# Performance work log

Hardware: AMD Instinct MI355X
Metric: run time of the kernel (lower is better)

Reference implementation:

```python
import jax, jax.numpy as jnp
import numpy as np

EMBED = 384
HEAD = 64


def setup_inputs() -> dict:
    key = jax.random.key(0)
    kx, kq, kk, kv = jax.random.split(key, 4)
    B, T = 4, 4096
    x = jax.random.normal(kx, (B, T, EMBED), dtype=jnp.float32)
    # torch Linear(384, 64, bias=False): weight (64, 384), y = x @ W.T.
    # Store pre-transposed as (EMBED, HEAD) so y = x @ W.
    s = 1.0 / np.sqrt(EMBED)  # kaiming-uniform-ish scale
    Wq = jax.random.uniform(kq, (EMBED, HEAD), jnp.float32, -s, s)
    Wk = jax.random.uniform(kk, (EMBED, HEAD), jnp.float32, -s, s)
    Wv = jax.random.uniform(kv, (EMBED, HEAD), jnp.float32, -s, s)
    return {"x": x, "Wq": Wq, "Wk": Wk, "Wv": Wv}


def reference(x, Wq, Wk, Wv):
    # q, k, v: [B, T, H]
    q = x @ Wq
    k = x @ Wk
    v = x @ Wv
    scale = k.shape[-1] ** (-0.5)
    scores = jnp.einsum("bth,bsh->bts", q, k) * scale  # [B, T, T]
    # Faithful to the original: tril, then mask anything equal to 0 with -inf
    # (this also masks exact zeros inside the causal region).
    tril = jnp.tril(scores)
    masked = jnp.where(tril == 0, -jnp.inf, tril)
    attn = jax.nn.softmax(masked, axis=-1)
    out = jnp.einsum("bts,bsh->bth", attn, v)  # [B, T, H]
    return out
```

## Files before the change

kernel.cpp:

```cpp
#include <hip/hip_runtime.h>
#include <hip/hip_bf16.h>
#include <stdint.h>


#define EMBED 384
#define HEAD  64
#define NB    4
#define NT    4096
#define NROWS (NB * NT)
#define MAXCH 16

#define SCALE_Q 0.18033688011112042f

typedef short bf16x8 __attribute__((ext_vector_type(8)));
typedef float f32x4  __attribute__((ext_vector_type(4)));

__device__ __forceinline__ unsigned short bfround(float f) {
    union { float f; unsigned u; } v; v.f = f;
    return (unsigned short)((v.u + 0x8000u) >> 16);
}
__device__ __forceinline__ unsigned packbf(float lo, float hi) {
    union { float f; unsigned u; } a, b; a.f = lo; b.f = hi;
    return ((a.u + 0x8000u) >> 16) | ((b.u + 0x8000u) & 0xFFFF0000u);
}

__global__ __launch_bounds__(256)
void wprep_kernel(const float* __restrict__ Wq,
                  const float* __restrict__ Wk,
                  const float* __restrict__ Wv,
                  unsigned short* __restrict__ Wt)
{
    int idx = blockIdx.x * 256 + threadIdx.x;
    int k = idx / 192;
    int n = idx - k * 192;
    int sel = n >> 6, nc = n & 63;
    const float* wp = (sel == 0) ? Wq : ((sel == 1) ? Wk : Wv);
    Wt[n * EMBED + k] = bfround(wp[(size_t)k * HEAD + nc]);
}

__global__ __launch_bounds__(256, 4)
void proj_kernel(const float* __restrict__ x,
                 const unsigned short* __restrict__ Wt,
                 unsigned short* __restrict__ Qo,
                 unsigned short* __restrict__ Ko,
                 unsigned short* __restrict__ Vto)
{
    __shared__ __attribute__((aligned(16))) unsigned short wsm[192][72];
    __shared__ __attribute__((aligned(16))) unsigned short xs[64][72];
    unsigned short (*vbuf)[72] = (unsigned short (*)[72])&xs[0][0];

    const int t    = threadIdx.x;
    const int w    = t >> 6;
    const int lane = t & 63;
    const int quad = lane >> 4;
    const int l16  = lane & 15;
    const int r0   = blockIdx.x * 64;

    f32x4 acc[12];
#pragma unroll
    for (int i = 0; i < 12; ++i) acc[i] = (f32x4){0.f, 0.f, 0.f, 0.f};

    const int wrow = t >> 3, wc = t & 7;
    const int xrow = t >> 4, xc = t & 15;

    for (int kc = 0; kc < 6; ++kc) {
        const int k0 = kc * 64;
        uint4 wr[6];
#pragma unroll
        for (int i = 0; i < 6; ++i)
            wr[i] = *(const uint4*)(Wt + (size_t)(wrow + i * 32) * EMBED + k0 + wc * 8);
        float4 xr[4];
#pragma unroll
        for (int i = 0; i < 4; ++i)
            xr[i] = *(const float4*)(x + (size_t)(r0 + xrow + i * 16) * EMBED + k0 + xc * 4);
        __syncthreads();
#pragma unroll
        for (int i = 0; i < 6; ++i)
            *(uint4*)&wsm[wrow + i * 32][wc * 8] = wr[i];
#pragma unroll
        for (int i = 0; i < 4; ++i) {
            uint2 pw; pw.x = packbf(xr[i].x, xr[i].y); pw.y = packbf(xr[i].z, xr[i].w);
            *(uint2*)&xs[xrow + i * 16][xc * 4] = pw;
        }
        __syncthreads();
#pragma unroll
        for (int ks = 0; ks < 2; ++ks) {
            bf16x8 a = *(const bf16x8*)&xs[w * 16 + l16][ks * 32 + quad * 8];
#pragma unroll
            for (int nt = 0; nt < 12; ++nt) {
                bf16x8 b = *(const bf16x8*)&wsm[nt * 16 + l16][ks * 32 + quad * 8];
                acc[nt] = __builtin_amdgcn_mfma_f32_16x16x32_bf16(a, b, acc[nt], 0, 0, 0);
            }
        }
    }

#pragma unroll
    for (int nt = 0; nt < 8; ++nt) {
        int col = (nt & 3) * 16 + l16;
#pragma unroll
        for (int r = 0; r < 4; ++r) {
            int row = r0 + w * 16 + quad * 4 + r;
            if (nt < 4) Qo[(size_t)row * HEAD + col] = bfround(acc[nt][r] * SCALE_Q);
            else        Ko[(size_t)row * HEAD + col] = bfround(acc[nt][r]);
        }
    }
    __syncthreads();
#pragma unroll
    for (int nt = 8; nt < 12; ++nt) {
        int d = (nt & 3) * 16 + l16;
#pragma unroll
        for (int r = 0; r < 4; ++r)
            vbuf[d][w * 16 + quad * 4 + r] = bfround(acc[nt][r]);
    }
    __syncthreads();
    {
        const int batch = r0 >> 12;
        const int s0 = r0 & (NT - 1);
#pragma unroll
        for (int i = 0; i < 2; ++i) {
            int idx = t + i * 256;
            int d = idx >> 3, c = idx & 7;
            *(uint4*)(Vto + ((size_t)(batch * HEAD + d)) * NT + s0 + c * 8) =
                *(const uint4*)&vbuf[d][c * 8];
        }
    }
}

__global__ __launch_bounds__(256, 6)
void attn_kernel(const unsigned short* __restrict__ Qi,
                 const unsigned short* __restrict__ Ki,
                 const unsigned short* __restrict__ Vti,
                 float* __restrict__ opart,
                 float* __restrict__ lpart)
{
    __shared__ __attribute__((aligned(16))) unsigned short Kt[64][64];
    __shared__ __attribute__((aligned(16))) unsigned short Vs[64][64];
    __shared__ __attribute__((aligned(16))) unsigned short Ps[4][16][72];

    const int t    = threadIdx.x;
    const int w    = t >> 6;
    const int lane = t & 63;
    const int quad = lane >> 4;
    const int l16  = lane & 15;
    const int sw   = l16 & 7;

    const int batch = blockIdx.x & 3;
    int bid = blockIdx.x >> 2;
    int m = 63;
    int nc = 16;
    while (bid >= nc) { bid -= nc; --m; nc = (m >> 2) + 1; }
    const int c = bid;
    const int kt0 = c * 4;
    const int ntiles = min(4, m + 1 - kt0);
    const int q0 = m * 64 + w * 16;

    const unsigned short* Kbg = Ki  + (size_t)batch * NT * HEAD;
    const unsigned short* Vbg = Vti + (size_t)batch * HEAD * NT;

    bf16x8 bq0, bq1;
    {
        const unsigned short* qp = Qi + (size_t)(batch * NT + q0 + l16) * HEAD + quad * 8;
        bq0 = *(const bf16x8*)(qp);
        bq1 = *(const bf16x8*)(qp + 32);
    }

    f32x4 o[4];
#pragma unroll
    for (int i = 0; i < 4; ++i) o[i] = (f32x4){0.f, 0.f, 0.f, 0.f};
    float rs = 0.f;

    const int srow0 = t >> 3, sc = t & 7;
    const int srow1 = srow0 + 32;
    const int scc0 = sc ^ (srow0 & 7);
    const int scc1 = sc ^ (srow1 & 7);

    uint4 kr0, kr1, vr0, vr1;
    kr0 = *(const uint4*)(Kbg + (size_t)(kt0 * 64 + srow0) * HEAD + sc * 8);
    kr1 = *(const uint4*)(Kbg + (size_t)(kt0 * 64 + srow1) * HEAD + sc * 8);
    vr0 = *(const uint4*)(Vbg + (size_t)srow0 * NT + kt0 * 64 + sc * 8);
    vr1 = *(const uint4*)(Vbg + (size_t)srow1 * NT + kt0 * 64 + sc * 8);

    for (int j = 0; j < ntiles; ++j) {
        const int kt = kt0 + j;
        __syncthreads();
        *(uint4*)&Kt[srow0][scc0 * 8] = kr0;
        *(uint4*)&Kt[srow1][scc1 * 8] = kr1;
        *(uint4*)&Vs[srow0][scc0 * 8] = vr0;
        *(uint4*)&Vs[srow1][scc1 * 8] = vr1;
        __syncthreads();
        if (j + 1 < ntiles) {
            const int nt4 = (kt + 1) * 64;
            kr0 = *(const uint4*)(Kbg + (size_t)(nt4 + srow0) * HEAD + sc * 8);
            kr1 = *(const uint4*)(Kbg + (size_t)(nt4 + srow1) * HEAD + sc * 8);
            vr0 = *(const uint4*)(Vbg + (size_t)srow0 * NT + nt4 + sc * 8);
            vr1 = *(const uint4*)(Vbg + (size_t)srow1 * NT + nt4 + sc * 8);
        }

        const bool diag = (kt == m);
#pragma unroll
        for (int ts = 0; ts < 4; ++ts) {
            bf16x8 ak0 = *(const bf16x8*)&Kt[ts * 16 + l16][(quad ^ sw) * 8];
            bf16x8 ak1 = *(const bf16x8*)&Kt[ts * 16 + l16][((4 + quad) ^ sw) * 8];
            f32x4 z = (f32x4){0.f, 0.f, 0.f, 0.f};
            z = __builtin_amdgcn_mfma_f32_16x16x32_bf16(ak0, bq0, z, 0, 0, 0);
            z = __builtin_amdgcn_mfma_f32_16x16x32_bf16(ak1, bq1, z, 0, 0, 0);
            float p[4];
#pragma unroll
            for (int r = 0; r < 4; ++r) {
                float pv = __builtin_amdgcn_exp2f(z[r]);
                if (diag) {
                    int sg = ts * 16 + quad * 4 + r;
                    int qg = w * 16 + l16;
                    pv = (sg > qg) ? 0.f : pv;
                }
                p[r] = pv;
            }
            rs += (p[0] + p[1]) + (p[2] + p[3]);
            uint2 pw; pw.x = packbf(p[0], p[1]); pw.y = packbf(p[2], p[3]);
            *(uint2*)&Ps[w][l16][ts * 16 + quad * 4] = pw;
        }
        bf16x8 ap0 = *(const bf16x8*)&Ps[w][l16][quad * 8];
        bf16x8 ap1 = *(const bf16x8*)&Ps[w][l16][32 + quad * 8];
#pragma unroll
        for (int nd = 0; nd < 4; ++nd) {
            bf16x8 av0 = *(const bf16x8*)&Vs[nd * 16 + l16][(quad ^ sw) * 8];
            bf16x8 av1 = *(const bf16x8*)&Vs[nd * 16 + l16][((4 + quad) ^ sw) * 8];
            o[nd] = __builtin_amdgcn_mfma_f32_16x16x32_bf16(ap0, av0, o[nd], 0, 0, 0);
            o[nd] = __builtin_amdgcn_mfma_f32_16x16x32_bf16(ap1, av1, o[nd], 0, 0, 0);
        }
    }

    rs += __shfl_xor(rs, 16, 64);
    rs += __shfl_xor(rs, 32, 64);
    if (quad == 0)
        lpart[(size_t)c * NROWS + batch * NT + q0 + l16] = rs;
    float* ob = opart + (size_t)c * NROWS * HEAD;
#pragma unroll
    for (int r = 0; r < 4; ++r) {
        size_t off = (size_t)(batch * NT + q0 + quad * 4 + r) * HEAD;
#pragma unroll
        for (int nd = 0; nd < 4; ++nd)
            ob[off + nd * 16 + l16] = o[nd][r];
    }
}

__global__ __launch_bounds__(256)
void combine_kernel(const float* __restrict__ opart,
                    const float* __restrict__ lpart,
                    float* __restrict__ out)
{
    int gid = blockIdx.x * 256 + threadIdx.x;
    int row = gid >> 4;
    int d4  = (gid & 15) * 4;
    int m   = (row & (NT - 1)) >> 6;
    int nch = (m >> 2) + 1;
    f32x4 a = (f32x4){0.f, 0.f, 0.f, 0.f};
    float l = 0.f;
    for (int cc = 0; cc < nch; ++cc) {
        a += *(const f32x4*)(opart + (size_t)cc * NROWS * HEAD + (size_t)row * HEAD + d4);
        l += lpart[(size_t)cc * NROWS + row];
    }
    float inv = 1.0f / l;
    a[0] *= inv; a[1] *= inv; a[2] *= inv; a[3] *= inv;
    *(f32x4*)(out + (size_t)row * HEAD + d4) = a;
}

extern "C" void kernel_launch(void* const* d_in, const int* in_sizes, int n_in,
                              void* d_out, int out_size, void* d_ws, size_t ws_size,
                              hipStream_t stream)
{
    const float* x  = (const float*)d_in[0];
    const float* Wq = (const float*)d_in[1];
    const float* Wk = (const float*)d_in[2];
    const float* Wv = (const float*)d_in[3];
    float* out = (float*)d_out;

    unsigned short* Qw  = (unsigned short*)d_ws;
    unsigned short* Kw  = Qw + (size_t)NROWS * HEAD;
    unsigned short* Vtw = Kw + (size_t)NROWS * HEAD;
    unsigned short* Wtw = Vtw + (size_t)NROWS * HEAD;
    float* opart = (float*)(Wtw + (size_t)192 * EMBED);
    float* lpart = opart + (size_t)MAXCH * NROWS * HEAD;

    wprep_kernel<<<(192 * EMBED) / 256, 256, 0, stream>>>(Wq, Wk, Wv, Wtw);
    proj_kernel<<<NROWS / 64, 256, 0, stream>>>(x, Wtw, Qw, Kw, Vtw);
    attn_kernel<<<4 * 544, 256, 0, stream>>>(Qw, Kw, Vtw, opart, lpart);
    combine_kernel<<<NROWS * 16 / 256, 256, 0, stream>>>(opart, lpart, out);
}
```

Baseline: 129.0 us.

## Process 128-row query tiles per block and store partial outputs in bf16

Each attention block now covers 128 query rows, with each wave handling two 16-row sub-tiles. K and V fragments are loaded from LDS once and reused for both sub-tiles, and the grid is halved. Partial output accumulators are written as bf16 instead of fp32 to cut split-K write and read traffic, and the combine kernel reads them with 8-wide loads. The cost is more registers per thread (occupancy hint lowered from 6 to 4), coarser causal work balance, and some precision loss in the partial sums.

Measured after the change: 206.4 us. 1.6x slower.

```diff
diff --git a/kernel.cpp b/kernel.cpp
--- a/kernel.cpp
+++ b/kernel.cpp
@@ -126,11 +126,11 @@
     }
 }
 
-__global__ __launch_bounds__(256, 6)
+__global__ __launch_bounds__(256, 4)
 void attn_kernel(const unsigned short* __restrict__ Qi,
                  const unsigned short* __restrict__ Ki,
                  const unsigned short* __restrict__ Vti,
-                 float* __restrict__ opart,
+                 unsigned short* __restrict__ opart,
                  float* __restrict__ lpart)
 {
     __shared__ __attribute__((aligned(16))) unsigned short Kt[64][64];
@@ -146,28 +146,31 @@
 
     const int batch = blockIdx.x & 3;
     int bid = blockIdx.x >> 2;
-    int m = 63;
-    int nc = 16;
-    while (bid >= nc) { bid -= nc; --m; nc = (m >> 2) + 1; }
+    int m = 31;
+    int nch = 16;
+    while (bid >= nch) { bid -= nch; --m; nch = (m + 2) >> 1; }
     const int c = bid;
     const int kt0 = c * 4;
-    const int ntiles = min(4, m + 1 - kt0);
-    const int q0 = m * 64 + w * 16;
+    const int ntiles = min(4, 2 * m + 2 - kt0);
+    const int qw = m * 128 + w * 32;
 
     const unsigned short* Kbg = Ki  + (size_t)batch * NT * HEAD;
     const unsigned short* Vbg = Vti + (size_t)batch * HEAD * NT;
 
-    bf16x8 bq0, bq1;
-    {
-        const unsigned short* qp = Qi + (size_t)(batch * NT + q0 + l16) * HEAD + quad * 8;
-        bq0 = *(const bf16x8*)(qp);
-        bq1 = *(const bf16x8*)(qp + 32);
-    }
-
-    f32x4 o[4];
-#pragma unroll
-    for (int i = 0; i < 4; ++i) o[i] = (f32x4){0.f, 0.f, 0.f, 0.f};
-    float rs = 0.f;
+    bf16x8 bq0[2], bq1[2];
+#pragma unroll
+    for (int qs = 0; qs < 2; ++qs) {
+        const unsigned short* qp = Qi + (size_t)(batch * NT + qw + qs * 16 + l16) * HEAD + quad * 8;
+        bq0[qs] = *(const bf16x8*)(qp);
+        bq1[qs] = *(const bf16x8*)(qp + 32);
+    }
+
+    f32x4 o[2][4];
+#pragma unroll
+    for (int a = 0; a < 2; ++a)
+#pragma unroll
+        for (int b = 0; b < 4; ++b) o[a][b] = (f32x4){0.f, 0.f, 0.f, 0.f};
+    float rs[2] = {0.f, 0.f};
 
     const int srow0 = t >> 3, sc = t & 7;
     const int srow1 = srow0 + 32;
@@ -196,73 +199,111 @@
             vr1 = *(const uint4*)(Vbg + (size_t)srow1 * NT + nt4 + sc * 8);
         }
 
-        const bool diag = (kt == m);
+        bf16x8 ak0[4], ak1[4], av0[4], av1[4];
 #pragma unroll
         for (int ts = 0; ts < 4; ++ts) {
-            bf16x8 ak0 = *(const bf16x8*)&Kt[ts * 16 + l16][(quad ^ sw) * 8];
-            bf16x8 ak1 = *(const bf16x8*)&Kt[ts * 16 + l16][((4 + quad) ^ sw) * 8];
-            f32x4 z = (f32x4){0.f, 0.f, 0.f, 0.f};
-            z = __builtin_amdgcn_mfma_f32_16x16x32_bf16(ak0, bq0, z, 0, 0, 0);
-            z = __builtin_amdgcn_mfma_f32_16x16x32_bf16(ak1, bq1, z, 0, 0, 0);
-            float p[4];
+            ak0[ts] = *(const bf16x8*)&Kt[ts * 16 + l16][(quad ^ sw) * 8];
+            ak1[ts] = *(const bf16x8*)&Kt[ts * 16 + l16][((4 + quad) ^ sw) * 8];
+        }
+#pragma unroll
+        for (int nd = 0; nd < 4; ++nd) {
+            av0[nd] = *(const bf16x8*)&Vs[nd * 16 + l16][(quad ^ sw) * 8];
+            av1[nd] = *(const bf16x8*)&Vs[nd * 16 + l16][((4 + quad) ^ sw) * 8];
+        }
+
+        const bool diag = (kt >= 2 * m);
+#pragma unroll
+        for (int qs = 0; qs < 2; ++qs) {
+            f32x4 z[4];
+#pragma unroll
+            for (int ts = 0; ts < 4; ++ts) {
+                f32x4 zz = (f32x4){0.f, 0.f, 0.f, 0.f};
+                zz = __builtin_amdgcn_mfma_f32_16x16x32_bf16(ak0[ts], bq0[qs], zz, 0, 0, 0);
+                zz = __builtin_amdgcn_mfma_f32_16x16x32_bf16(ak1[ts], bq1[qs], zz, 0, 0, 0);
+                z[ts] = zz;
+            }
+            const int qg = qw + qs * 16 + l16;
+#pragma unroll
+            for (int ts = 0; ts < 4; ++ts) {
+                float p[4];
+#pragma unroll
+                for (int r = 0; r < 4; ++r) {
+                    float pv = __builtin_amdgcn_exp2f(z[ts][r]);
+                    if (diag) {
+                        int sg = kt * 64 + ts * 16 + quad * 4 + r;
+                        pv = (sg > qg) ? 0.f : pv;
+                    }
+                    p[r] = pv;
+                }
+                rs[qs] += (p[0] + p[1]) + (p[2] + p[3]);
+                uint2 pw; pw.x = packbf(p[0], p[1]); pw.y = packbf(p[2], p[3]);
+                *(uint2*)&Ps[w][l16][ts * 16 + quad * 4] = pw;
+            }
+            bf16x8 ap0 = *(const bf16x8*)&Ps[w][l16][quad * 8];
+            bf16x8 ap1 = *(const bf16x8*)&Ps[w][l16][32 + quad * 8];
+#pragma unroll
+            for (int nd = 0; nd < 4; ++nd) {
+                o[qs][nd] = __builtin_amdgcn_mfma_f32_16x16x32_bf16(ap0, av0[nd], o[qs][nd], 0, 0, 0);
+                o[qs][nd] = __builtin_amdgcn_mfma_f32_16x16x32_bf16(ap1, av1[nd], o[qs][nd], 0, 0, 0);
+            }
+        }
+    }
+
+#pragma unroll
+    for (int qs = 0; qs < 2; ++qs) {
+        float vs = rs[qs];
+        vs += __shfl_xor(vs, 16, 64);
+        vs += __shfl_xor(vs, 32, 64);
+        if (quad == 0)
+            lpart[(size_t)c * NROWS + batch * NT + qw + qs * 16 + l16] = vs;
+    }
+    unsigned short* ob = opart + (size_t)c * NROWS * HEAD + (size_t)batch * NT * HEAD;
+#pragma unroll
+    for (int qs = 0; qs < 2; ++qs)
+#pragma unroll
+        for (int nd = 0; nd < 4; ++nd)
 #pragma unroll
             for (int r = 0; r < 4; ++r) {
-                float pv = __builtin_amdgcn_exp2f(z[r]);
-                if (diag) {
-                    int sg = ts * 16 + quad * 4 + r;
-                    int qg = w * 16 + l16;
-                    pv = (sg > qg) ? 0.f : pv;
+                float own = o[qs][nd][r];
+                float oth = __shfl_xor(own, 1, 64);
+                unsigned u = (lane & 1) ? packbf(oth, own) : packbf(own, oth);
+                if (!(lane & 1)) {
+                    int row = qw + qs * 16 + quad * 4 + r;
+                    *(unsigned*)&ob[(size_t)row * HEAD + nd * 16 + l16] = u;
                 }
-                p[r] = pv;
-            }
-            rs += (p[0] + p[1]) + (p[2] + p[3]);
-            uint2 pw; pw.x = packbf(p[0], p[1]); pw.y = packbf(p[2], p[3]);
-            *(uint2*)&Ps[w][l16][ts * 16 + quad * 4] = pw;
-        }
-        bf16x8 ap0 = *(const bf16x8*)&Ps[w][l16][quad * 8];
-        bf16x8 ap1 = *(const bf16x8*)&Ps[w][l16][32 + quad * 8];
-#pragma unroll
-        for (int nd = 0; nd < 4; ++nd) {
-            bf16x8 av0 = *(const bf16x8*)&Vs[nd * 16 + l16][(quad ^ sw) * 8];
-            bf16x8 av1 = *(const bf16x8*)&Vs[nd * 16 + l16][((4 + quad) ^ sw) * 8];
-            o[nd] = __builtin_amdgcn_mfma_f32_16x16x32_bf16(ap0, av0, o[nd], 0, 0, 0);
-            o[nd] = __builtin_amdgcn_mfma_f32_16x16x32_bf16(ap1, av1, o[nd], 0, 0, 0);
-        }
-    }
-
-    rs += __shfl_xor(rs, 16, 64);
-    rs += __shfl_xor(rs, 32, 64);
-    if (quad == 0)
-        lpart[(size_t)c * NROWS + batch * NT + q0 + l16] = rs;
-    float* ob = opart + (size_t)c * NROWS * HEAD;
-#pragma unroll
-    for (int r = 0; r < 4; ++r) {
-        size_t off = (size_t)(batch * NT + q0 + quad * 4 + r) * HEAD;
-#pragma unroll
-        for (int nd = 0; nd < 4; ++nd)
-            ob[off + nd * 16 + l16] = o[nd][r];
-    }
+            }
 }
 
 __global__ __launch_bounds__(256)
-void combine_kernel(const float* __restrict__ opart,
+void combine_kernel(const unsigned short* __restrict__ opart,
                     const float* __restrict__ lpart,
                     float* __restrict__ out)
 {
     int gid = blockIdx.x * 256 + threadIdx.x;
-    int row = gid >> 4;
-    int d4  = (gid & 15) * 4;
-    int m   = (row & (NT - 1)) >> 6;
-    int nch = (m >> 2) + 1;
-    f32x4 a = (f32x4){0.f, 0.f, 0.f, 0.f};
+    int row = gid >> 3;
+    int d8  = (gid & 7) * 8;
+    int m   = (row & (NT - 1)) >> 7;
+    int nch = (m + 2) >> 1;
+    float acc[8] = {0.f, 0.f, 0.f, 0.f, 0.f, 0.f, 0.f, 0.f};
     float l = 0.f;
     for (int cc = 0; cc < nch; ++cc) {
-        a += *(const f32x4*)(opart + (size_t)cc * NROWS * HEAD + (size_t)row * HEAD + d4);
+        const unsigned short* p = opart + (size_t)cc * NROWS * HEAD + (size_t)row * HEAD + d8;
+        uint4 u = *(const uint4*)p;
+        union { unsigned u; float f; } cv;
+#pragma unroll
+        for (int i = 0; i < 4; ++i) {
+            unsigned ui = (i == 0) ? u.x : (i == 1) ? u.y : (i == 2) ? u.z : u.w;
+            cv.u = ui << 16;          acc[i * 2]     += cv.f;
+            cv.u = ui & 0xFFFF0000u;  acc[i * 2 + 1] += cv.f;
+        }
         l += lpart[(size_t)cc * NROWS + row];
     }
     float inv = 1.0f / l;
-    a[0] *= inv; a[1] *= inv; a[2] *= inv; a[3] *= inv;
-    *(f32x4*)(out + (size_t)row * HEAD + d4) = a;
+    float4 r0, r1;
+    r0.x = acc[0] * inv; r0.y = acc[1] * inv; r0.z = acc[2] * inv; r0.w = acc[3] * inv;
+    r1.x = acc[4] * inv; r1.y = acc[5] * inv; r1.z = acc[6] * inv; r1.w = acc[7] * inv;
+    *(float4*)(out + (size_t)row * HEAD + d8)     = r0;
+    *(float4*)(out + (size_t)row * HEAD + d8 + 4) = r1;
 }
 
 extern "C" void kernel_launch(void* const* d_in, const int* in_sizes, int n_in,
@@ -279,11 +320,11 @@
     unsigned short* Kw  = Qw + (size_t)NROWS * HEAD;
     unsigned short* Vtw = Kw + (size_t)NROWS * HEAD;
     unsigned short* Wtw = Vtw + (size_t)NROWS * HEAD;
-    float* opart = (float*)(Wtw + (size_t)192 * EMBED);
-    float* lpart = opart + (size_t)MAXCH * NROWS * HEAD;
+    unsigned short* opart = Wtw + (size_t)192 * EMBED;
+    float* lpart = (float*)(opart + (size_t)MAXCH * NROWS * HEAD);
 
     wprep_kernel<<<(192 * EMBED) / 256, 256, 0, stream>>>(Wq, Wk, Wv, Wtw);
     proj_kernel<<<NROWS / 64, 256, 0, stream>>>(x, Wtw, Qw, Kw, Vtw);
-    attn_kernel<<<4 * 544, 256, 0, stream>>>(Qw, Kw, Vtw, opart, lpart);
-    combine_kernel<<<NROWS * 16 / 256, 256, 0, stream>>>(opart, lpart, out);
-}
+    attn_kernel<<<4 * 272, 256, 0, stream>>>(Qw, Kw, Vtw, opart, lpart);
+    combine_kernel<<<NROWS * 8 / 256, 256, 0, stream>>>(opart, lpart, out);
+}
```
